# Kernel tuning notes

Hardware: AMD Instinct MI355X
Metric: run time of the kernel (lower is better)

## Reference

```python
import jax, jax.numpy as jnp
import numpy as np

D_MODEL = 512
DFF = 2048
E = 8
K = 2
B, N = 2, 2048


def setup_inputs() -> dict:
    key = jax.random.key(0)
    ks = jax.random.split(key, 6)
    x = jax.random.normal(ks[0], (B, N, D_MODEL), dtype=jnp.float32)
    # router: nn.Linear(d_model, E, bias=False), init normal(std=0.01), weight [E, d]
    router_w = jax.random.normal(ks[1], (E, D_MODEL), dtype=jnp.float32) * 0.01
    # expert linear1.weight [dff, d], linear2.weight [d, dff], xavier-uniform; biases zero in torch init,
    # but use small random biases so the backward test exercises their grads meaningfully.
    lim1 = float(np.sqrt(6.0 / (D_MODEL + DFF)))
    w1_all = jax.random.uniform(ks[2], (E, DFF, D_MODEL), minval=-lim1, maxval=lim1, dtype=jnp.float32)
    w2_all = jax.random.uniform(ks[3], (E, D_MODEL, DFF), minval=-lim1, maxval=lim1, dtype=jnp.float32)
    b1_all = jax.random.normal(ks[4], (E, DFF), dtype=jnp.float32) * 0.01
    b2_all = jax.random.normal(ks[5], (E, D_MODEL), dtype=jnp.float32) * 0.01
    return {"x": x, "router_w": router_w, "w1_all": w1_all, "b1_all": b1_all,
            "w2_all": w2_all, "b2_all": b2_all}


def reference(x, router_w, w1_all, b1_all, w2_all, b2_all):
    Bb, Nn, C = x.shape
    L = Bb * Nn
    x_flat = x.reshape(L, C)

    # Router: logits -> softmax -> top-k -> renormalized weights
    router_logits = x_flat @ router_w.T                      # [L, E]
    router_probs = jax.nn.softmax(router_logits, axis=-1)
    expert_weights, expert_indices = jax.lax.top_k(router_probs, K)  # [L, K]
    expert_weights = expert_weights / (jnp.sum(expert_weights, axis=-1, keepdims=True) + 1e-9)

    # Dense per-expert MLP (same math as per-token gathered bmm; dropout in eval = identity)
    h = jax.nn.relu(jnp.einsum('lc,efc->lef', x_flat, w1_all) + b1_all[None])  # [L, E, dff]
    out_all = jnp.einsum('lef,ecf->lec', h, w2_all) + b2_all[None]             # [L, E, C]

    # Gather selected experts' outputs and combine
    out_sel = jnp.take_along_axis(out_all, expert_indices[:, :, None], axis=1)  # [L, K, C]
    final = jnp.sum(out_sel * expert_weights[:, :, None], axis=1)               # [L, C]
    return final.reshape(Bb, Nn, C)
```

## Files before the change

kernel.cpp:

```cpp
#include <hip/hip_runtime.h>

#define D_MODEL 512
#define DFF 2048
#define NEXP 8
#define LTOK 4096
#define NPAIR 8192
#define PMAX 9216
#define MAXT 72

#define HD_COUNTS 0
#define HD_CURSOR 8
#define HD_OFF    16
#define HD_NTILES 25
#define HD_TILE_E 32
#define HD_TILE_R 112

typedef __attribute__((ext_vector_type(8))) short bf16x8;
typedef __attribute__((ext_vector_type(4))) float f32x4;

__device__ __forceinline__ unsigned short f2bf(float f){
  unsigned u = __builtin_bit_cast(unsigned, f);
  u += 0x7fffu + ((u>>16)&1u);
  return (unsigned short)(u>>16);
}

__global__ void router_top2(const float* __restrict__ x, const float* __restrict__ rw,
                            int* __restrict__ pair_e, float* __restrict__ pair_w){
  int t = blockIdx.x;
  int l = threadIdx.x;
  const float* xr = x + (size_t)t*D_MODEL;
  float xv[8];
  #pragma unroll
  for (int j=0;j<8;j++) xv[j] = xr[j*64+l];
  double lg[NEXP];
  #pragma unroll
  for (int e=0;e<NEXP;e++){
    const float* we = rw + e*D_MODEL;
    double s = 0.0;
    #pragma unroll
    for (int j=0;j<8;j++) s += (double)xv[j] * (double)we[j*64+l];
    #pragma unroll
    for (int off=32; off; off>>=1) s += __shfl_xor(s, off);
    lg[e] = s;
  }
  if (l==0){
    double mx = lg[0];
    #pragma unroll
    for (int e=1;e<NEXP;e++) if (lg[e]>mx) mx = lg[e];
    double p[NEXP], sum = 0.0;
    #pragma unroll
    for (int e=0;e<NEXP;e++){ p[e] = exp(lg[e]-mx); sum += p[e]; }
    #pragma unroll
    for (int e=0;e<NEXP;e++) p[e] /= sum;
    int i0 = 0;
    for (int e=1;e<NEXP;e++) if (p[e] > p[i0]) i0 = e;
    int i1 = (i0==0) ? 1 : 0;
    for (int e=0;e<NEXP;e++){ if (e==i0) continue; if (p[e] > p[i1]) i1 = e; }
    double s2 = p[i0] + p[i1] + 1e-9;
    pair_e[2*t]   = i0;  pair_e[2*t+1] = i1;
    pair_w[2*t]   = (float)(p[i0]/s2);
    pair_w[2*t+1] = (float)(p[i1]/s2);
  }
}

__global__ void count_kernel(const int* __restrict__ pair_e, int* __restrict__ hdr){
  __shared__ int cnt[NEXP];
  int tid = threadIdx.x;
  if (tid < NEXP) cnt[tid] = 0;
  __syncthreads();
  int base = blockIdx.x*1024;
  #pragma unroll
  for (int i=0;i<4;i++) atomicAdd(&cnt[pair_e[base + i*256 + tid]], 1);
  __syncthreads();
  if (tid < NEXP) atomicAdd(&hdr[HD_COUNTS+tid], cnt[tid]);
}

__global__ void plan_kernel(int* __restrict__ hdr, int* __restrict__ gtok,
                            int* __restrict__ gtk){
  if (threadIdx.x==0){
    int off=0, nt=0;
    for (int e=0;e<NEXP;e++){
      hdr[HD_OFF+e]=off;
      int c = hdr[HD_COUNTS+e];
      int tiles = (c+127)>>7;
      for (int i=0;i<tiles;i++){ hdr[HD_TILE_E+nt]=e; hdr[HD_TILE_R+nt]=off+(i<<7); nt++; }
      off += tiles<<7;
    }
    hdr[HD_OFF+NEXP]=off;
    hdr[HD_NTILES]=nt;
  }
  for (int i=threadIdx.x; i<PMAX; i+=blockDim.x){ gtok[i]=0; gtk[i]=-1; }
}

__global__ void assign_kernel(const int* __restrict__ pair_e, int* __restrict__ hdr,
                              int* __restrict__ gtok, int* __restrict__ gtk){
  __shared__ int cnt[NEXP];
  __shared__ int base[NEXP];
  int tid = threadIdx.x;
  if (tid < NEXP) cnt[tid] = 0;
  __syncthreads();
  int id = blockIdx.x*256 + tid;
  int e = pair_e[id];
  int myrank = atomicAdd(&cnt[e], 1);
  __syncthreads();
  if (tid < NEXP) base[tid] = atomicAdd(&hdr[HD_CURSOR+tid], cnt[tid]);
  __syncthreads();
  int row = hdr[HD_OFF+e] + base[e] + myrank;
  gtok[row] = id>>1;
  gtk[row]  = id;
}

__global__ void gather_x_kernel(const float* __restrict__ x, const int* __restrict__ gtok,
                                unsigned short* __restrict__ xg){
  int id = blockIdx.x*256 + threadIdx.x;
  if (id >= PMAX*(D_MODEL/8)) return;
  int row = id>>6, j = id&63;
  int t = gtok[row];
  const float4* s = (const float4*)(x + (size_t)t*D_MODEL + j*8);
  float4 a = s[0], b = s[1];
  uint4 o;
  o.x = (unsigned)f2bf(a.x) | ((unsigned)f2bf(a.y)<<16);
  o.y = (unsigned)f2bf(a.z) | ((unsigned)f2bf(a.w)<<16);
  o.z = (unsigned)f2bf(b.x) | ((unsigned)f2bf(b.y)<<16);
  o.w = (unsigned)f2bf(b.z) | ((unsigned)f2bf(b.w)<<16);
  *(uint4*)(xg + (size_t)id*8) = o;
}

__global__ void convw_kernel(const float* __restrict__ w1, const float* __restrict__ w2,
                             unsigned short* __restrict__ w1b, unsigned short* __restrict__ w2b){
  int id = blockIdx.x*256 + threadIdx.x;
  const int per = NEXP*DFF*D_MODEL/8;
  const float* src; unsigned short* dst; int k;
  if (id < per){ src = w1; dst = w1b; k = id; }
  else         { src = w2; dst = w2b; k = id - per; }
  const float4* s = (const float4*)(src + (size_t)k*8);
  float4 a = s[0], b = s[1];
  uint4 o;
  o.x = (unsigned)f2bf(a.x) | ((unsigned)f2bf(a.y)<<16);
  o.y = (unsigned)f2bf(a.z) | ((unsigned)f2bf(a.w)<<16);
  o.z = (unsigned)f2bf(b.x) | ((unsigned)f2bf(b.y)<<16);
  o.w = (unsigned)f2bf(b.z) | ((unsigned)f2bf(b.w)<<16);
  *(uint4*)(dst + (size_t)k*8) = o;
}

template<int NDIM, int KDIM, int MODE>
__global__ __launch_bounds__(256,2) void gemm_moe(
    const unsigned short* __restrict__ A,
    const unsigned short* __restrict__ Bw,
    const float* __restrict__ bias,
    unsigned short* __restrict__ outH,
    float* __restrict__ outO,
    const float* __restrict__ pair_w,
    const int* __restrict__ hdr,
    const int* __restrict__ gtk)
{
  __shared__ __align__(16) unsigned short As[128*64];
  __shared__ __align__(16) unsigned short Bs[128*64];
  int bx = blockIdx.x;
  if (bx >= hdr[HD_NTILES]) return;
  int e    = hdr[HD_TILE_E+bx];
  int row0 = hdr[HD_TILE_R+bx];
  int n0   = blockIdx.y<<7;
  int tid  = threadIdx.x;
  int w = tid>>6, l = tid&63;
  int wm = w>>1, wn = w&1;

  const unsigned short* Ag = A  + (size_t)row0*KDIM;
  const unsigned short* Bg = Bw + (size_t)e*NDIM*KDIM + (size_t)n0*KDIM;

  f32x4 acc[4][4];
  f32x4 zz = {0.f,0.f,0.f,0.f};
  #pragma unroll
  for (int i=0;i<4;i++)
    #pragma unroll
    for (int j=0;j<4;j++) acc[i][j] = zz;

  int srow = (w<<3) + (l>>3);
  int c8   = l&7;
  char* AsB = (char*)As;
  char* BsB = (char*)Bs;

  for (int kt=0; kt<KDIM/64; ++kt){
    #pragma unroll
    for (int i=0;i<4;i++){
      int r  = i*32 + srow;
      int sc = (c8 ^ (r&7))*8;
      const unsigned short* ga = Ag + (size_t)r*KDIM + kt*64 + sc;
      const unsigned short* gb = Bg + (size_t)r*KDIM + kt*64 + sc;
      int ldso = i*4096 + w*1024 + l*16;
      __builtin_amdgcn_global_load_lds((const __attribute__((address_space(1))) void*)ga,
                                       (__attribute__((address_space(3))) void*)(AsB + ldso), 16, 0, 0);
      __builtin_amdgcn_global_load_lds((const __attribute__((address_space(1))) void*)gb,
                                       (__attribute__((address_space(3))) void*)(BsB + ldso), 16, 0, 0);
    }
    __syncthreads();
    #pragma unroll
    for (int kk=0;kk<2;kk++){
      bf16x8 av[4], bv[4];
      #pragma unroll
      for (int mi=0;mi<4;mi++){
        int r  = (wm<<6) + (mi<<4) + (l&15);
        int ch = ((kk<<2) + (l>>4)) ^ (r&7);
        av[mi] = *(const bf16x8*)(AsB + r*128 + ch*16);
      }
      #pragma unroll
      for (int ni=0;ni<4;ni++){
        int r  = (wn<<6) + (ni<<4) + (l&15);
        int ch = ((kk<<2) + (l>>4)) ^ (r&7);
        bv[ni] = *(const bf16x8*)(BsB + r*128 + ch*16);
      }
      #pragma unroll
      for (int mi=0;mi<4;mi++)
        #pragma unroll
        for (int ni=0;ni<4;ni++)
          acc[mi][ni] = __builtin_amdgcn_mfma_f32_16x16x32_bf16(av[mi], bv[ni], acc[mi][ni], 0,0,0);
    }
    __syncthreads();
  }

  int lc = l&15, lq = l>>4;
  #pragma unroll
  for (int ni=0;ni<4;ni++){
    int col = n0 + (wn<<6) + (ni<<4) + lc;
    float bcol = bias[e*NDIM + col];
    #pragma unroll
    for (int mi=0;mi<4;mi++){
      int rbase = row0 + (wm<<6) + (mi<<4) + lq*4;
      #pragma unroll
      for (int q=0;q<4;q++){
        int gr = rbase + q;
        float v = acc[mi][ni][q] + bcol;
        if (MODE==0){
          v = v>0.f ? v : 0.f;
          outH[(size_t)gr*NDIM + col] = f2bf(v);
        } else {
          int tk = gtk[gr];
          if (tk>=0){
            float wgt = pair_w[tk];
            atomicAdd(&outO[(size_t)(tk>>1)*D_MODEL + col], wgt*v);
          }
        }
      }
    }
  }
}

extern "C" void kernel_launch(void* const* d_in, const int* in_sizes, int n_in,
                              void* d_out, int out_size, void* d_ws, size_t ws_size,
                              hipStream_t stream){
  const float* x  = (const float*)d_in[0];
  const float* rw = (const float*)d_in[1];
  const float* w1 = (const float*)d_in[2];
  const float* b1 = (const float*)d_in[3];
  const float* w2 = (const float*)d_in[4];
  const float* b2 = (const float*)d_in[5];
  float* out = (float*)d_out;

  const size_t OFF_HDR  = 0;
  const size_t OFF_PE   = 1024;
  const size_t OFF_PW   = 66560;
  const size_t OFF_GTOK = 99328;
  const size_t OFF_GTK  = 136192;
  const size_t OFF_XG   = 180224;
  const size_t OFF_W1B  = OFF_XG  + (size_t)PMAX*D_MODEL*2;
  const size_t OFF_W2B  = OFF_W1B + (size_t)NEXP*DFF*D_MODEL*2;
  const size_t OFF_H    = OFF_W2B + (size_t)NEXP*DFF*D_MODEL*2;
  const size_t WS_NEED  = OFF_H   + (size_t)PMAX*DFF*2;
  if (ws_size < WS_NEED) return;

  char* ws = (char*)d_ws;
  int*   hdr    = (int*)(ws + OFF_HDR);
  int*   pair_e = (int*)(ws + OFF_PE);
  float* pair_w = (float*)(ws + OFF_PW);
  int*   gtok   = (int*)(ws + OFF_GTOK);
  int*   gtk    = (int*)(ws + OFF_GTK);
  unsigned short* xg  = (unsigned short*)(ws + OFF_XG);
  unsigned short* w1b = (unsigned short*)(ws + OFF_W1B);
  unsigned short* w2b = (unsigned short*)(ws + OFF_W2B);
  unsigned short* h   = (unsigned short*)(ws + OFF_H);

  hipMemsetAsync(hdr, 0, 1024, stream);
  hipMemsetAsync(out, 0, (size_t)LTOK*D_MODEL*sizeof(float), stream);
  router_top2<<<LTOK, 64, 0, stream>>>(x, rw, pair_e, pair_w);
  count_kernel<<<NPAIR/1024, 256, 0, stream>>>(pair_e, hdr);
  plan_kernel<<<1, 256, 0, stream>>>(hdr, gtok, gtk);
  assign_kernel<<<NPAIR/256, 256, 0, stream>>>(pair_e, hdr, gtok, gtk);
  gather_x_kernel<<<(PMAX*64)/256, 256, 0, stream>>>(x, gtok, xg);
  convw_kernel<<<8192, 256, 0, stream>>>(w1, w2, w1b, w2b);
  gemm_moe<DFF, D_MODEL, 0><<<dim3(MAXT,16), 256, 0, stream>>>(xg, w1b, b1, h, nullptr, nullptr, hdr, gtk);
  gemm_moe<D_MODEL, DFF, 1><<<dim3(MAXT,4), 256, 0, stream>>>(h, w2b, b2, nullptr, out, pair_w, hdr, gtk);
}
```

Baseline: 154.0 us.

## Double-buffer MoE GEMM LDS loads and split second GEMM into 64-row tiles

The two expert GEMMs now use double-buffered LDS staging: the next k-tile's global-to-LDS loads are issued before computing the current one, with raw barriers and vmcnt waits in place of __syncthreads. Blocks are launched as a 1D grid with a swizzled tile order to group work across the N dimension. The second GEMM switches to 64-row M tiles so more workgroups run along its short N dimension. The cost is twice the LDS per block, which may limit occupancy, and hand-written waitcnt logic that must match the number of outstanding loads.

```diff
diff --git a/kernel.cpp b/kernel.cpp
--- a/kernel.cpp
+++ b/kernel.cpp
@@ -23,6 +23,13 @@
   u += 0x7fffu + ((u>>16)&1u);
   return (unsigned short)(u>>16);
 }
+
+template<int N> __device__ __forceinline__ void wait_vm(){
+  if constexpr (N==8)      asm volatile("s_waitcnt vmcnt(8)" ::: "memory");
+  else if constexpr (N==6) asm volatile("s_waitcnt vmcnt(6)" ::: "memory");
+  else                     asm volatile("s_waitcnt vmcnt(0)" ::: "memory");
+}
+#define RAW_BARRIER() asm volatile("s_barrier" ::: "memory")
 
 __global__ void router_top2(const float* __restrict__ x, const float* __restrict__ rw,
                             int* __restrict__ pair_e, float* __restrict__ pair_w){
@@ -143,8 +150,8 @@
   *(uint4*)(dst + (size_t)k*8) = o;
 }
 
-template<int NDIM, int KDIM, int MODE>
-__global__ __launch_bounds__(256,2) void gemm_moe(
+template<int MT, int NDIM, int KDIM, int MODE>
+__global__ __launch_bounds__(256,2) void gemm2p(
     const unsigned short* __restrict__ A,
     const unsigned short* __restrict__ Bw,
     const float* __restrict__ bias,
@@ -154,74 +161,117 @@
     const int* __restrict__ hdr,
     const int* __restrict__ gtk)
 {
-  __shared__ __align__(16) unsigned short As[128*64];
-  __shared__ __align__(16) unsigned short Bs[128*64];
-  int bx = blockIdx.x;
-  if (bx >= hdr[HD_NTILES]) return;
-  int e    = hdr[HD_TILE_E+bx];
-  int row0 = hdr[HD_TILE_R+bx];
-  int n0   = blockIdx.y<<7;
-  int tid  = threadIdx.x;
+  constexpr int NT_N = NDIM/128;
+  constexpr int MAXM = (MT==128) ? MAXT : 2*MAXT;
+  constexpr int NWG  = MAXM*NT_N;
+  constexpr int WC   = (MT==128) ? 64 : 32;
+  constexpr int FN   = WC/16;
+  constexpr int LPT  = MT/32 + 4;
+  constexpr int ABYT = MT*128;
+  constexpr int NTK  = KDIM/64;
+
+  __shared__ __align__(16) unsigned short As[2*MT*64];
+  __shared__ __align__(16) unsigned short Bs[2*128*64];
+
+  int wg  = blockIdx.x;
+  int swz = (wg & 7)*(NWG/8) + (wg >> 3);
+  int m   = swz / NT_N;
+  int n0  = (swz % NT_N) << 7;
+
+  int ntiles = hdr[HD_NTILES];
+  int e, row0;
+  if constexpr (MT==128){
+    if (m >= ntiles) return;
+    e = hdr[HD_TILE_E+m];  row0 = hdr[HD_TILE_R+m];
+  } else {
+    if (m >= 2*ntiles) return;
+    e = hdr[HD_TILE_E+(m>>1)];  row0 = hdr[HD_TILE_R+(m>>1)] + ((m&1)<<6);
+  }
+
+  int tid = threadIdx.x;
   int w = tid>>6, l = tid&63;
-  int wm = w>>1, wn = w&1;
+  int wm = (MT==128) ? (w>>1) : 0;
+  int wn = (MT==128) ? (w&1)  : w;
 
   const unsigned short* Ag = A  + (size_t)row0*KDIM;
   const unsigned short* Bg = Bw + (size_t)e*NDIM*KDIM + (size_t)n0*KDIM;
 
-  f32x4 acc[4][4];
+  f32x4 acc[4][FN];
   f32x4 zz = {0.f,0.f,0.f,0.f};
   #pragma unroll
   for (int i=0;i<4;i++)
     #pragma unroll
-    for (int j=0;j<4;j++) acc[i][j] = zz;
+    for (int j=0;j<FN;j++) acc[i][j] = zz;
 
   int srow = (w<<3) + (l>>3);
   int c8   = l&7;
   char* AsB = (char*)As;
   char* BsB = (char*)Bs;
 
-  for (int kt=0; kt<KDIM/64; ++kt){
+  auto stage = [&](int b, int kt){
+    #pragma unroll
+    for (int i=0;i<MT/32;i++){
+      int r  = i*32 + srow;
+      int sc = (c8 ^ (r&7))*8;
+      const unsigned short* ga = Ag + (size_t)r*KDIM + kt*64 + sc;
+      int ldso = b*ABYT + i*4096 + w*1024 + l*16;
+      __builtin_amdgcn_global_load_lds((const __attribute__((address_space(1))) void*)ga,
+                                       (__attribute__((address_space(3))) void*)(AsB + ldso), 16, 0, 0);
+    }
     #pragma unroll
     for (int i=0;i<4;i++){
       int r  = i*32 + srow;
       int sc = (c8 ^ (r&7))*8;
-      const unsigned short* ga = Ag + (size_t)r*KDIM + kt*64 + sc;
       const unsigned short* gb = Bg + (size_t)r*KDIM + kt*64 + sc;
-      int ldso = i*4096 + w*1024 + l*16;
-      __builtin_amdgcn_global_load_lds((const __attribute__((address_space(1))) void*)ga,
-                                       (__attribute__((address_space(3))) void*)(AsB + ldso), 16, 0, 0);
+      int ldso = b*16384 + i*4096 + w*1024 + l*16;
       __builtin_amdgcn_global_load_lds((const __attribute__((address_space(1))) void*)gb,
                                        (__attribute__((address_space(3))) void*)(BsB + ldso), 16, 0, 0);
     }
-    __syncthreads();
+  };
+
+  auto compute = [&](int b){
     #pragma unroll
     for (int kk=0;kk<2;kk++){
-      bf16x8 av[4], bv[4];
+      bf16x8 av[4], bv[FN];
       #pragma unroll
       for (int mi=0;mi<4;mi++){
         int r  = (wm<<6) + (mi<<4) + (l&15);
         int ch = ((kk<<2) + (l>>4)) ^ (r&7);
-        av[mi] = *(const bf16x8*)(AsB + r*128 + ch*16);
+        av[mi] = *(const bf16x8*)(AsB + b*ABYT + r*128 + ch*16);
       }
       #pragma unroll
-      for (int ni=0;ni<4;ni++){
-        int r  = (wn<<6) + (ni<<4) + (l&15);
+      for (int ni=0;ni<FN;ni++){
+        int r  = wn*WC + (ni<<4) + (l&15);
         int ch = ((kk<<2) + (l>>4)) ^ (r&7);
-        bv[ni] = *(const bf16x8*)(BsB + r*128 + ch*16);
+        bv[ni] = *(const bf16x8*)(BsB + b*16384 + r*128 + ch*16);
       }
       #pragma unroll
       for (int mi=0;mi<4;mi++)
         #pragma unroll
-        for (int ni=0;ni<4;ni++)
+        for (int ni=0;ni<FN;ni++)
           acc[mi][ni] = __builtin_amdgcn_mfma_f32_16x16x32_bf16(av[mi], bv[ni], acc[mi][ni], 0,0,0);
     }
-    __syncthreads();
-  }
+  };
+
+  stage(0, 0);
+  int cur = 0;
+  for (int kt=0; kt<NTK-1; ++kt){
+    stage(cur^1, kt+1);
+    wait_vm<LPT>();
+    RAW_BARRIER();
+    compute(cur);
+    asm volatile("s_waitcnt lgkmcnt(0)" ::: "memory");
+    RAW_BARRIER();
+    cur ^= 1;
+  }
+  wait_vm<0>();
+  RAW_BARRIER();
+  compute(cur);
 
   int lc = l&15, lq = l>>4;
   #pragma unroll
-  for (int ni=0;ni<4;ni++){
-    int col = n0 + (wn<<6) + (ni<<4) + lc;
+  for (int ni=0;ni<FN;ni++){
+    int col = n0 + wn*WC + (ni<<4) + lc;
     float bcol = bias[e*NDIM + col];
     #pragma unroll
     for (int mi=0;mi<4;mi++){
@@ -287,6 +337,6 @@
   assign_kernel<<<NPAIR/256, 256, 0, stream>>>(pair_e, hdr, gtok, gtk);
   gather_x_kernel<<<(PMAX*64)/256, 256, 0, stream>>>(x, gtok, xg);
   convw_kernel<<<8192, 256, 0, stream>>>(w1, w2, w1b, w2b);
-  gemm_moe<DFF, D_MODEL, 0><<<dim3(MAXT,16), 256, 0, stream>>>(xg, w1b, b1, h, nullptr, nullptr, hdr, gtk);
-  gemm_moe<D_MODEL, DFF, 1><<<dim3(MAXT,4), 256, 0, stream>>>(h, w2b, b2, nullptr, out, pair_w, hdr, gtk);
-}
+  gemm2p<128, DFF, D_MODEL, 0><<<MAXT*16, 256, 0, stream>>>(xg, w1b, b1, h, nullptr, nullptr, hdr, gtk);
+  gemm2p<64, D_MODEL, DFF, 1><<<2*MAXT*4, 256, 0, stream>>>(h, w2b, b2, nullptr, out, pair_w, hdr, gtk);
+}
```

Result: faster. 127.7 us (-17.1%).
